# Kernel tuning notes

Hardware: AMD Instinct MI355X
Metric: run time of the kernel (lower is better)

## Reference

```python
import jax, jax.numpy as jnp
import numpy as np


def squash(t, axis=-1):
    sq = jnp.sum(t * t, axis=axis, keepdims=True)
    scale = sq / (1.0 + sq)
    return scale * t / jnp.sqrt(sq + 1e-8)


def setup_inputs() -> dict:
    key = jax.random.key(0)
    k1, k2 = jax.random.split(key)
    B, in_caps, out_caps, in_dim, out_dim = 128, 2048, 32, 8, 16
    x = jax.random.normal(k1, (B, in_caps, in_dim), dtype=jnp.float32)
    W = jax.random.normal(k2, (in_caps, out_caps, in_dim, out_dim), dtype=jnp.float32)
    return {"x": x, "W": W}


def reference(x, W):
    # x: [B, in_caps, in_dim], W: [in_caps, out_caps, in_dim, out_dim]
    # u_hat: [B, in_caps, out_caps, out_dim]
    u_hat = jnp.einsum('bni,noid->bnod', x, W)
    B, in_caps, out_caps, _ = u_hat.shape
    b = jnp.zeros((B, in_caps, out_caps, 1), dtype=u_hat.dtype)
    v = None
    for i in range(3):
        c = jax.nn.softmax(b, axis=2)              # over out_caps
        s = jnp.sum(c * u_hat, axis=1)             # [B, out_caps, out_dim]
        v = squash(s)                              # [B, out_caps, out_dim]
        if i < 2:
            b = b + jnp.sum(u_hat * v[:, None], axis=-1, keepdims=True)
    return v
```

## Files before the change

### kernel.cpp

```cpp
#include <hip/hip_runtime.h>


constexpr int NC = 2048;
constexpr int OC = 32;
constexpr int OD = 16;

typedef const __attribute__((address_space(1))) void* gas1_t;
typedef __attribute__((address_space(3))) void* las3_t;

__device__ __forceinline__ void gld16(const void* g, void* l) {
    __builtin_amdgcn_global_load_lds((gas1_t)g, (las3_t)l, 16, 0, 0);
}

#define MEMFENCE() asm volatile("" ::: "memory")
#define BAR() do { MEMFENCE(); __builtin_amdgcn_s_barrier(); MEMFENCE(); } while (0)

template<bool FIRST, bool ATOMIC>
__global__ __launch_bounds__(256)
__attribute__((amdgpu_waves_per_eu(2, 2)))
void caps_pass(const float* __restrict__ xg, const float* __restrict__ Wg,
               const float* __restrict__ vin, float* __restrict__ pout)
{
    __shared__ float4 Wl[2][1024];
    __shared__ float4 xl[1024];

    const int tid  = threadIdx.x;
    const int bid  = blockIdx.x;
    const int nsup = (bid & 7) | ((bid >> 6) << 3);
    const int bt   = (bid >> 3) & 7;
    const int w    = __builtin_amdgcn_readfirstlane(tid >> 6);
    const int lane = tid & 63;
    const int o    = lane & 31;
    const int h    = lane >> 5;
    const int sw   = o & 7;
    const int b0   = bt * 16 + w * 4;
    const int nbase = nsup * 32;

    const float4* Wg4 = (const float4*)Wg;
    const float4* xg4 = (const float4*)xg;

    float4 acc[4][2];
#pragma unroll
    for (int r = 0; r < 4; ++r)
#pragma unroll
        for (int qq = 0; qq < 2; ++qq) acc[r][qq] = make_float4(0.f, 0.f, 0.f, 0.f);

    float4 vr[4][2];
    if (!FIRST) {
        const float4* v4 = (const float4*)vin;
#pragma unroll
        for (int r = 0; r < 4; ++r)
#pragma unroll
            for (int qq = 0; qq < 2; ++qq)
                vr[r][qq] = v4[(size_t)(b0 + r) * 128 + o * 4 + h * 2 + qq];
    }

#pragma unroll
    for (int j = 0; j < 4; ++j) {
        const int L = tid + 256 * j;
        const int n = L >> 5, bb = (L >> 1) & 15, k = L & 1;
        gld16(&xg4[(size_t)(bt * 16 + bb) * 4096 + (size_t)(nbase + n) * 2 + k], &xl[L]);
    }
#pragma unroll
    for (int j = 0; j < 4; ++j) {
        const int L = tid + 256 * j;
        const int oo = L >> 5, cc = L & 31;
        gld16(&Wg4[(size_t)nbase * 1024 + oo * 32 + (cc ^ (oo & 7))], &Wl[0][L]);
    }

#pragma unroll 1
    for (int t = 0; t < 32; ++t) {
        if (t < 31) {
#pragma unroll
            for (int j = 0; j < 4; ++j) {
                const int L = tid + 256 * j;
                const int oo = L >> 5, cc = L & 31;
                gld16(&Wg4[(size_t)(nbase + t + 1) * 1024 + oo * 32 + (cc ^ (oo & 7))],
                      &Wl[(t + 1) & 1][L]);
            }
            asm volatile("s_waitcnt vmcnt(4)" ::: "memory");
        } else {
            asm volatile("s_waitcnt vmcnt(0)" ::: "memory");
        }
        BAR();

        float xr[4][8];
#pragma unroll
        for (int r = 0; r < 4; ++r) {
            const float4 xa = xl[t * 32 + (w * 4 + r) * 2 + 0];
            const float4 xb = xl[t * 32 + (w * 4 + r) * 2 + 1];
            xr[r][0] = xa.x; xr[r][1] = xa.y; xr[r][2] = xa.z; xr[r][3] = xa.w;
            xr[r][4] = xb.x; xr[r][5] = xb.y; xr[r][6] = xb.z; xr[r][7] = xb.w;
        }
        const float4* wrow = &Wl[t & 1][o * 32];

        if (FIRST) {
#pragma unroll
            for (int i = 0; i < 8; ++i)
#pragma unroll
                for (int qq = 0; qq < 2; ++qq) {
                    const float4 wv = wrow[(i * 4 + h * 2 + qq) ^ sw];
#pragma unroll
                    for (int r = 0; r < 4; ++r) {
                        acc[r][qq].x = fmaf(xr[r][i], wv.x, acc[r][qq].x);
                        acc[r][qq].y = fmaf(xr[r][i], wv.y, acc[r][qq].y);
                        acc[r][qq].z = fmaf(xr[r][i], wv.z, acc[r][qq].z);
                        acc[r][qq].w = fmaf(xr[r][i], wv.w, acc[r][qq].w);
                    }
                }
        } else {
            float4 u[4][2];
#pragma unroll
            for (int r = 0; r < 4; ++r)
#pragma unroll
                for (int qq = 0; qq < 2; ++qq) u[r][qq] = make_float4(0.f, 0.f, 0.f, 0.f);
#pragma unroll
            for (int i = 0; i < 8; ++i)
#pragma unroll
                for (int qq = 0; qq < 2; ++qq) {
                    const float4 wv = wrow[(i * 4 + h * 2 + qq) ^ sw];
#pragma unroll
                    for (int r = 0; r < 4; ++r) {
                        u[r][qq].x = fmaf(xr[r][i], wv.x, u[r][qq].x);
                        u[r][qq].y = fmaf(xr[r][i], wv.y, u[r][qq].y);
                        u[r][qq].z = fmaf(xr[r][i], wv.z, u[r][qq].z);
                        u[r][qq].w = fmaf(xr[r][i], wv.w, u[r][qq].w);
                    }
                }
#pragma unroll
            for (int r = 0; r < 4; ++r) {
                float tp = 0.f;
#pragma unroll
                for (int qq = 0; qq < 2; ++qq) {
                    tp = fmaf(u[r][qq].x, vr[r][qq].x, tp);
                    tp = fmaf(u[r][qq].y, vr[r][qq].y, tp);
                    tp = fmaf(u[r][qq].z, vr[r][qq].z, tp);
                    tp = fmaf(u[r][qq].w, vr[r][qq].w, tp);
                }
                const float tt = tp + __shfl_xor(tp, 32);
                const float e = __expf(tt);
                float Z = e;
                Z += __shfl_xor(Z, 1);
                Z += __shfl_xor(Z, 2);
                Z += __shfl_xor(Z, 4);
                Z += __shfl_xor(Z, 8);
                Z += __shfl_xor(Z, 16);
                const float c = e / Z;
#pragma unroll
                for (int qq = 0; qq < 2; ++qq) {
                    acc[r][qq].x = fmaf(c, u[r][qq].x, acc[r][qq].x);
                    acc[r][qq].y = fmaf(c, u[r][qq].y, acc[r][qq].y);
                    acc[r][qq].z = fmaf(c, u[r][qq].z, acc[r][qq].z);
                    acc[r][qq].w = fmaf(c, u[r][qq].w, acc[r][qq].w);
                }
            }
        }
        BAR();
    }

    const float sc = FIRST ? (1.0f / 32.0f) : 1.0f;
    if (ATOMIC) {
#pragma unroll
        for (int r = 0; r < 4; ++r) {
            float* sb = pout + (size_t)(b0 + r) * (OC * OD) + o * OD + h * 8;
#pragma unroll
            for (int qq = 0; qq < 2; ++qq) {
                atomicAdd(sb + qq * 4 + 0, acc[r][qq].x * sc);
                atomicAdd(sb + qq * 4 + 1, acc[r][qq].y * sc);
                atomicAdd(sb + qq * 4 + 2, acc[r][qq].z * sc);
                atomicAdd(sb + qq * 4 + 3, acc[r][qq].w * sc);
            }
        }
    } else {
        float4* P4 = (float4*)pout;
#pragma unroll
        for (int r = 0; r < 4; ++r) {
            const size_t base = ((size_t)(nsup * 128 + b0 + r) * 4 + h * 2) * 32 + o;
#pragma unroll
            for (int qq = 0; qq < 2; ++qq) {
                float4 v;
                v.x = acc[r][qq].x * sc; v.y = acc[r][qq].y * sc;
                v.z = acc[r][qq].z * sc; v.w = acc[r][qq].w * sc;
                P4[base + (size_t)qq * 32] = v;
            }
        }
    }
}

__global__ void reduce_squash(const float* __restrict__ P, const float* __restrict__ vprev,
                              float* __restrict__ vout)
{
    __shared__ float sqb[256];
    const int tid = threadIdx.x;
    const int blk = blockIdx.x;
    const float4* P4 = (const float4*)P;

    float4 a = make_float4(0.f, 0.f, 0.f, 0.f);
#pragma unroll 4
    for (int ns = 0; ns < 64; ++ns) {
        const float4 p = P4[(size_t)ns * 16384 + blk * 256 + tid];
        a.x += p.x; a.y += p.y; a.z += p.z; a.w += p.w;
    }
    sqb[tid] = a.x * a.x + a.y * a.y + a.z * a.z + a.w * a.w;
    __syncthreads();
    const int base = tid & 0x9F;
    const float sq = sqb[base] + sqb[base + 32] + sqb[base + 64] + sqb[base + 96];
    const float f = sq / ((1.0f + sq) * sqrtf(sq + 1e-8f));

    const int b  = blk * 2 + (tid >> 7);
    const int hq = (tid >> 5) & 3;
    const int o  = tid & 31;
    const size_t unit = (size_t)(b * 32 + o) * 4 + hq;
    float4 r;
    r.x = a.x * f; r.y = a.y * f; r.z = a.z * f; r.w = a.w * f;
    if (vprev) {
        const float4 p = ((const float4*)vprev)[unit];
        r.x += p.x; r.y += p.y; r.z += p.z; r.w += p.w;
    }
    ((float4*)vout)[unit] = r;
}

__global__ void squash_k(const float* __restrict__ s, const float* __restrict__ vprev,
                         float* __restrict__ vout)
{
    const int row = blockIdx.x * blockDim.x + threadIdx.x;
    if (row >= 128 * 32) return;
    const float4* s4 = (const float4*)s;
    float4 t[4];
    float sq = 0.f;
#pragma unroll
    for (int q = 0; q < 4; ++q) {
        t[q] = s4[row * 4 + q];
        sq += t[q].x * t[q].x + t[q].y * t[q].y + t[q].z * t[q].z + t[q].w * t[q].w;
    }
    const float f = sq / ((1.0f + sq) * sqrtf(sq + 1e-8f));
    float4* o4 = (float4*)vout;
#pragma unroll
    for (int q = 0; q < 4; ++q) {
        float4 r;
        r.x = t[q].x * f; r.y = t[q].y * f; r.z = t[q].z * f; r.w = t[q].w * f;
        if (vprev) {
            const float4 p = ((const float4*)vprev)[row * 4 + q];
            r.x += p.x; r.y += p.y; r.z += p.z; r.w += p.w;
        }
        o4[row * 4 + q] = r;
    }
}

extern "C" void kernel_launch(void* const* d_in, const int* in_sizes, int n_in,
                              void* d_out, int out_size, void* d_ws, size_t ws_size,
                              hipStream_t stream)
{
    const float* x = (const float*)d_in[0];
    const float* W = (const float*)d_in[1];
    float* out = (float*)d_out;

    const size_t P_FLOATS = (size_t)64 * 128 * 4 * 32 * 4;
    const size_t NEED = (P_FLOATS + 2 * 65536) * sizeof(float);

    if (ws_size >= NEED) {
        float* P  = (float*)d_ws;
        float* v0 = P + P_FLOATS;
        float* vs = v0 + 65536;

        caps_pass<true, false><<<dim3(512), dim3(256), 0, stream>>>(x, W, nullptr, P);
        reduce_squash<<<dim3(64), dim3(256), 0, stream>>>(P, nullptr, v0);

        caps_pass<false, false><<<dim3(512), dim3(256), 0, stream>>>(x, W, v0, P);
        reduce_squash<<<dim3(64), dim3(256), 0, stream>>>(P, v0, vs);

        caps_pass<false, false><<<dim3(512), dim3(256), 0, stream>>>(x, W, vs, P);
        reduce_squash<<<dim3(64), dim3(256), 0, stream>>>(P, nullptr, out);
    } else {
        float* s  = (float*)d_ws;
        float* v0 = s + 65536;
        float* vs = v0 + 65536;
        const size_t sbytes = (size_t)65536 * sizeof(float);

        hipMemsetAsync(s, 0, sbytes, stream);
        caps_pass<true, true><<<dim3(512), dim3(256), 0, stream>>>(x, W, nullptr, s);
        squash_k<<<dim3(16), dim3(256), 0, stream>>>(s, nullptr, v0);

        hipMemsetAsync(s, 0, sbytes, stream);
        caps_pass<false, true><<<dim3(512), dim3(256), 0, stream>>>(x, W, v0, s);
        squash_k<<<dim3(16), dim3(256), 0, stream>>>(s, v0, vs);

        hipMemsetAsync(s, 0, sbytes, stream);
        caps_pass<false, true><<<dim3(512), dim3(256), 0, stream>>>(x, W, vs, s);
        squash_k<<<dim3(16), dim3(256), 0, stream>>>(s, nullptr, out);
    }
}
```

Measured before the change: 195.3 us.

## Split input-capsule loop across two wave groups with LDS reduction

Doubles the block to 512 threads, with the two halves of the waves each processing alternate input capsules from a 4-deep W ring buffer. This halves the per-wave serial loop length and doubles the waves in flight, aiming to hide LDS/global latency. Partial accumulators are combined through LDS scratch before the store. This adds an extra barrier per iteration, a final reduction, higher LDS use and removes the waves_per_eu hint. The reduce kernel's unroll also goes from 4 to 8.

```diff
diff --git a/kernel.cpp b/kernel.cpp
--- a/kernel.cpp
+++ b/kernel.cpp
@@ -16,12 +16,11 @@
 #define BAR() do { MEMFENCE(); __builtin_amdgcn_s_barrier(); MEMFENCE(); } while (0)
 
 template<bool FIRST, bool ATOMIC>
-__global__ __launch_bounds__(256)
-__attribute__((amdgpu_waves_per_eu(2, 2)))
+__global__ __launch_bounds__(512)
 void caps_pass(const float* __restrict__ xg, const float* __restrict__ Wg,
                const float* __restrict__ vin, float* __restrict__ pout)
 {
-    __shared__ float4 Wl[2][1024];
+    __shared__ float4 Wl[4][1024];
     __shared__ float4 xl[1024];
 
     const int tid  = threadIdx.x;
@@ -29,11 +28,13 @@
     const int nsup = (bid & 7) | ((bid >> 6) << 3);
     const int bt   = (bid >> 3) & 7;
     const int w    = __builtin_amdgcn_readfirstlane(tid >> 6);
+    const int wg   = w & 3;
+    const int par  = w >> 2;
     const int lane = tid & 63;
     const int o    = lane & 31;
     const int h    = lane >> 5;
     const int sw   = o & 7;
-    const int b0   = bt * 16 + w * 4;
+    const int b0   = bt * 16 + wg * 4;
     const int nbase = nsup * 32;
 
     const float4* Wg4 = (const float4*)Wg;
@@ -56,27 +57,31 @@
     }
 
 #pragma unroll
-    for (int j = 0; j < 4; ++j) {
-        const int L = tid + 256 * j;
+    for (int j = 0; j < 2; ++j) {
+        const int L = tid + 512 * j;
         const int n = L >> 5, bb = (L >> 1) & 15, k = L & 1;
         gld16(&xg4[(size_t)(bt * 16 + bb) * 4096 + (size_t)(nbase + n) * 2 + k], &xl[L]);
     }
 #pragma unroll
     for (int j = 0; j < 4; ++j) {
-        const int L = tid + 256 * j;
-        const int oo = L >> 5, cc = L & 31;
-        gld16(&Wg4[(size_t)nbase * 1024 + oo * 32 + (cc ^ (oo & 7))], &Wl[0][L]);
+        const int L = tid + 512 * j;
+        const int cn = L >> 10, u = L & 1023;
+        const int oo = u >> 5, cc = u & 31;
+        gld16(&Wg4[(size_t)(nbase + cn) * 1024 + oo * 32 + (cc ^ (oo & 7))], &Wl[cn][u]);
     }
 
 #pragma unroll 1
-    for (int t = 0; t < 32; ++t) {
-        if (t < 31) {
+    for (int s = 0; s < 16; ++s) {
+        BAR();
+        if (s < 15) {
+            const int c0 = 2 * (s + 1);
 #pragma unroll
             for (int j = 0; j < 4; ++j) {
-                const int L = tid + 256 * j;
-                const int oo = L >> 5, cc = L & 31;
-                gld16(&Wg4[(size_t)(nbase + t + 1) * 1024 + oo * 32 + (cc ^ (oo & 7))],
-                      &Wl[(t + 1) & 1][L]);
+                const int L = tid + 512 * j;
+                const int cn = L >> 10, u = L & 1023;
+                const int oo = u >> 5, cc = u & 31;
+                gld16(&Wg4[(size_t)(nbase + c0 + cn) * 1024 + oo * 32 + (cc ^ (oo & 7))],
+                      &Wl[(c0 + cn) & 3][u]);
             }
             asm volatile("s_waitcnt vmcnt(4)" ::: "memory");
         } else {
@@ -84,15 +89,16 @@
         }
         BAR();
 
+        const int t = 2 * s + par;
         float xr[4][8];
 #pragma unroll
         for (int r = 0; r < 4; ++r) {
-            const float4 xa = xl[t * 32 + (w * 4 + r) * 2 + 0];
-            const float4 xb = xl[t * 32 + (w * 4 + r) * 2 + 1];
+            const float4 xa = xl[t * 32 + (wg * 4 + r) * 2 + 0];
+            const float4 xb = xl[t * 32 + (wg * 4 + r) * 2 + 1];
             xr[r][0] = xa.x; xr[r][1] = xa.y; xr[r][2] = xa.z; xr[r][3] = xa.w;
             xr[r][4] = xb.x; xr[r][5] = xb.y; xr[r][6] = xb.z; xr[r][7] = xb.w;
         }
-        const float4* wrow = &Wl[t & 1][o * 32];
+        const float4* wrow = &Wl[t & 3][o * 32];
 
         if (FIRST) {
 #pragma unroll
@@ -155,33 +161,51 @@
                 }
             }
         }
-        BAR();
-    }
-
-    const float sc = FIRST ? (1.0f / 32.0f) : 1.0f;
-    if (ATOMIC) {
-#pragma unroll
-        for (int r = 0; r < 4; ++r) {
-            float* sb = pout + (size_t)(b0 + r) * (OC * OD) + o * OD + h * 8;
+    }
+
+    BAR();
+    float4* scratch = (float4*)Wl;
+    if (par == 1) {
+#pragma unroll
+        for (int r = 0; r < 4; ++r)
+#pragma unroll
+            for (int qq = 0; qq < 2; ++qq)
+                scratch[wg * 512 + lane * 8 + ((r * 2 + qq) ^ (lane & 7))] = acc[r][qq];
+        asm volatile("s_waitcnt lgkmcnt(0)" ::: "memory");
+    }
+    BAR();
+    if (par == 0) {
+        const float sc = FIRST ? (1.0f / 32.0f) : 1.0f;
+#pragma unroll
+        for (int r = 0; r < 4; ++r)
 #pragma unroll
             for (int qq = 0; qq < 2; ++qq) {
-                atomicAdd(sb + qq * 4 + 0, acc[r][qq].x * sc);
-                atomicAdd(sb + qq * 4 + 1, acc[r][qq].y * sc);
-                atomicAdd(sb + qq * 4 + 2, acc[r][qq].z * sc);
-                atomicAdd(sb + qq * 4 + 3, acc[r][qq].w * sc);
-            }
-        }
-    } else {
-        float4* P4 = (float4*)pout;
-#pragma unroll
-        for (int r = 0; r < 4; ++r) {
-            const size_t base = ((size_t)(nsup * 128 + b0 + r) * 4 + h * 2) * 32 + o;
-#pragma unroll
-            for (int qq = 0; qq < 2; ++qq) {
-                float4 v;
-                v.x = acc[r][qq].x * sc; v.y = acc[r][qq].y * sc;
-                v.z = acc[r][qq].z * sc; v.w = acc[r][qq].w * sc;
-                P4[base + (size_t)qq * 32] = v;
+                const float4 p = scratch[wg * 512 + lane * 8 + ((r * 2 + qq) ^ (lane & 7))];
+                acc[r][qq].x = (acc[r][qq].x + p.x) * sc;
+                acc[r][qq].y = (acc[r][qq].y + p.y) * sc;
+                acc[r][qq].z = (acc[r][qq].z + p.z) * sc;
+                acc[r][qq].w = (acc[r][qq].w + p.w) * sc;
+            }
+        if (ATOMIC) {
+#pragma unroll
+            for (int r = 0; r < 4; ++r) {
+                float* sb = pout + (size_t)(b0 + r) * (OC * OD) + o * OD + h * 8;
+#pragma unroll
+                for (int qq = 0; qq < 2; ++qq) {
+                    atomicAdd(sb + qq * 4 + 0, acc[r][qq].x);
+                    atomicAdd(sb + qq * 4 + 1, acc[r][qq].y);
+                    atomicAdd(sb + qq * 4 + 2, acc[r][qq].z);
+                    atomicAdd(sb + qq * 4 + 3, acc[r][qq].w);
+                }
+            }
+        } else {
+            float4* P4 = (float4*)pout;
+#pragma unroll
+            for (int r = 0; r < 4; ++r) {
+                const size_t base = ((size_t)(nsup * 128 + b0 + r) * 4 + h * 2) * 32 + o;
+#pragma unroll
+                for (int qq = 0; qq < 2; ++qq)
+                    P4[base + (size_t)qq * 32] = acc[r][qq];
             }
         }
     }
@@ -196,7 +220,7 @@
     const float4* P4 = (const float4*)P;
 
     float4 a = make_float4(0.f, 0.f, 0.f, 0.f);
-#pragma unroll 4
+#pragma unroll 8
     for (int ns = 0; ns < 64; ++ns) {
         const float4 p = P4[(size_t)ns * 16384 + blk * 256 + tid];
         a.x += p.x; a.y += p.y; a.z += p.z; a.w += p.w;
@@ -263,13 +287,13 @@
         float* v0 = P + P_FLOATS;
         float* vs = v0 + 65536;
 
-        caps_pass<true, false><<<dim3(512), dim3(256), 0, stream>>>(x, W, nullptr, P);
+        caps_pass<true, false><<<dim3(512), dim3(512), 0, stream>>>(x, W, nullptr, P);
         reduce_squash<<<dim3(64), dim3(256), 0, stream>>>(P, nullptr, v0);
 
-        caps_pass<false, false><<<dim3(512), dim3(256), 0, stream>>>(x, W, v0, P);
+        caps_pass<false, false><<<dim3(512), dim3(512), 0, stream>>>(x, W, v0, P);
         reduce_squash<<<dim3(64), dim3(256), 0, stream>>>(P, v0, vs);
 
-        caps_pass<false, false><<<dim3(512), dim3(256), 0, stream>>>(x, W, vs, P);
+        caps_pass<false, false><<<dim3(512), dim3(512), 0, stream>>>(x, W, vs, P);
         reduce_squash<<<dim3(64), dim3(256), 0, stream>>>(P, nullptr, out);
     } else {
         float* s  = (float*)d_ws;
@@ -278,15 +302,15 @@
         const size_t sbytes = (size_t)65536 * sizeof(float);
 
         hipMemsetAsync(s, 0, sbytes, stream);
-        caps_pass<true, true><<<dim3(512), dim3(256), 0, stream>>>(x, W, nullptr, s);
+        caps_pass<true, true><<<dim3(512), dim3(512), 0, stream>>>(x, W, nullptr, s);
         squash_k<<<dim3(16), dim3(256), 0, stream>>>(s, nullptr, v0);
 
         hipMemsetAsync(s, 0, sbytes, stream);
-        caps_pass<false, true><<<dim3(512), dim3(256), 0, stream>>>(x, W, v0, s);
+        caps_pass<false, true><<<dim3(512), dim3(512), 0, stream>>>(x, W, v0, s);
         squash_k<<<dim3(16), dim3(256), 0, stream>>>(s, v0, vs);
 
         hipMemsetAsync(s, 0, sbytes, stream);
-        caps_pass<false, true><<<dim3(512), dim3(256), 0, stream>>>(x, W, vs, s);
+        caps_pass<false, true><<<dim3(512), dim3(512), 0, stream>>>(x, W, vs, s);
         squash_k<<<dim3(16), dim3(256), 0, stream>>>(s, nullptr, out);
     }
 }
```

Measured after the change: 214.5 us. +9.9%, slower.

## Halve capsules per block, read x directly from global, reprioritize waves

Applied to the files above, without the earlier changes.

Templates the capsule pass on capsules-per-block (NR=16), doubling the grid to 1024 blocks with a wider partial-sum buffer and a 128-way reduction. The x tile is no longer staged in LDS and is read per thread from global memory. The barrier is moved to the top of each iteration, s_setprio raises wave priority during the FMA phase, and the fixed waves_per_eu attribute is dropped. The aim is more occupancy and parallelism, at the cost of more partial-sum traffic and uncoalesced x loads.

```diff
diff --git a/kernel.cpp b/kernel.cpp
--- a/kernel.cpp
+++ b/kernel.cpp
@@ -15,29 +15,27 @@
 #define MEMFENCE() asm volatile("" ::: "memory")
 #define BAR() do { MEMFENCE(); __builtin_amdgcn_s_barrier(); MEMFENCE(); } while (0)
 
-template<bool FIRST, bool ATOMIC>
+template<int NR, bool FIRST, bool ATOMIC>
 __global__ __launch_bounds__(256)
-__attribute__((amdgpu_waves_per_eu(2, 2)))
 void caps_pass(const float* __restrict__ xg, const float* __restrict__ Wg,
                const float* __restrict__ vin, float* __restrict__ pout)
 {
     __shared__ float4 Wl[2][1024];
-    __shared__ float4 xl[1024];
-
+
+    constexpr int NSUPC = 2048 / NR;
     const int tid  = threadIdx.x;
     const int bid  = blockIdx.x;
-    const int nsup = (bid & 7) | ((bid >> 6) << 3);
-    const int bt   = (bid >> 3) & 7;
+    const int bt   = bid / NSUPC;
+    const int nsup = bid % NSUPC;
     const int w    = __builtin_amdgcn_readfirstlane(tid >> 6);
     const int lane = tid & 63;
     const int o    = lane & 31;
     const int h    = lane >> 5;
     const int sw   = o & 7;
     const int b0   = bt * 16 + w * 4;
-    const int nbase = nsup * 32;
+    const int nbase = nsup * NR;
 
     const float4* Wg4 = (const float4*)Wg;
-    const float4* xg4 = (const float4*)xg;
 
     float4 acc[4][2];
 #pragma unroll
@@ -55,12 +53,6 @@
                 vr[r][qq] = v4[(size_t)(b0 + r) * 128 + o * 4 + h * 2 + qq];
     }
 
-#pragma unroll
-    for (int j = 0; j < 4; ++j) {
-        const int L = tid + 256 * j;
-        const int n = L >> 5, bb = (L >> 1) & 15, k = L & 1;
-        gld16(&xg4[(size_t)(bt * 16 + bb) * 4096 + (size_t)(nbase + n) * 2 + k], &xl[L]);
-    }
 #pragma unroll
     for (int j = 0; j < 4; ++j) {
         const int L = tid + 256 * j;
@@ -69,8 +61,9 @@
     }
 
 #pragma unroll 1
-    for (int t = 0; t < 32; ++t) {
-        if (t < 31) {
+    for (int t = 0; t < NR; ++t) {
+        BAR();
+        if (t + 1 < NR) {
 #pragma unroll
             for (int j = 0; j < 4; ++j) {
                 const int L = tid + 256 * j;
@@ -84,16 +77,17 @@
         }
         BAR();
 
-        float xr[4][8];
+        const int n = nbase + t;
+        float xs[4][8];
 #pragma unroll
         for (int r = 0; r < 4; ++r) {
-            const float4 xa = xl[t * 32 + (w * 4 + r) * 2 + 0];
-            const float4 xb = xl[t * 32 + (w * 4 + r) * 2 + 1];
-            xr[r][0] = xa.x; xr[r][1] = xa.y; xr[r][2] = xa.z; xr[r][3] = xa.w;
-            xr[r][4] = xb.x; xr[r][5] = xb.y; xr[r][6] = xb.z; xr[r][7] = xb.w;
+            const float* xp = xg + ((size_t)(b0 + r) * NC + n) * 8;
+#pragma unroll
+            for (int i = 0; i < 8; ++i) xs[r][i] = xp[i];
         }
         const float4* wrow = &Wl[t & 1][o * 32];
 
+        __builtin_amdgcn_s_setprio(1);
         if (FIRST) {
 #pragma unroll
             for (int i = 0; i < 8; ++i)
@@ -102,10 +96,10 @@
                     const float4 wv = wrow[(i * 4 + h * 2 + qq) ^ sw];
 #pragma unroll
                     for (int r = 0; r < 4; ++r) {
-                        acc[r][qq].x = fmaf(xr[r][i], wv.x, acc[r][qq].x);
-                        acc[r][qq].y = fmaf(xr[r][i], wv.y, acc[r][qq].y);
-                        acc[r][qq].z = fmaf(xr[r][i], wv.z, acc[r][qq].z);
-                        acc[r][qq].w = fmaf(xr[r][i], wv.w, acc[r][qq].w);
+                        acc[r][qq].x = fmaf(xs[r][i], wv.x, acc[r][qq].x);
+                        acc[r][qq].y = fmaf(xs[r][i], wv.y, acc[r][qq].y);
+                        acc[r][qq].z = fmaf(xs[r][i], wv.z, acc[r][qq].z);
+                        acc[r][qq].w = fmaf(xs[r][i], wv.w, acc[r][qq].w);
                     }
                 }
         } else {
@@ -121,10 +115,10 @@
                     const float4 wv = wrow[(i * 4 + h * 2 + qq) ^ sw];
 #pragma unroll
                     for (int r = 0; r < 4; ++r) {
-                        u[r][qq].x = fmaf(xr[r][i], wv.x, u[r][qq].x);
-                        u[r][qq].y = fmaf(xr[r][i], wv.y, u[r][qq].y);
-                        u[r][qq].z = fmaf(xr[r][i], wv.z, u[r][qq].z);
-                        u[r][qq].w = fmaf(xr[r][i], wv.w, u[r][qq].w);
+                        u[r][qq].x = fmaf(xs[r][i], wv.x, u[r][qq].x);
+                        u[r][qq].y = fmaf(xs[r][i], wv.y, u[r][qq].y);
+                        u[r][qq].z = fmaf(xs[r][i], wv.z, u[r][qq].z);
+                        u[r][qq].w = fmaf(xs[r][i], wv.w, u[r][qq].w);
                     }
                 }
 #pragma unroll
@@ -155,7 +149,7 @@
                 }
             }
         }
-        BAR();
+        __builtin_amdgcn_s_setprio(0);
     }
 
     const float sc = FIRST ? (1.0f / 32.0f) : 1.0f;
@@ -187,6 +181,7 @@
     }
 }
 
+template<int NS>
 __global__ void reduce_squash(const float* __restrict__ P, const float* __restrict__ vprev,
                               float* __restrict__ vout)
 {
@@ -196,8 +191,8 @@
     const float4* P4 = (const float4*)P;
 
     float4 a = make_float4(0.f, 0.f, 0.f, 0.f);
-#pragma unroll 4
-    for (int ns = 0; ns < 64; ++ns) {
+#pragma unroll 8
+    for (int ns = 0; ns < NS; ++ns) {
         const float4 p = P4[(size_t)ns * 16384 + blk * 256 + tid];
         a.x += p.x; a.y += p.y; a.z += p.z; a.w += p.w;
     }
@@ -255,22 +250,37 @@
     const float* W = (const float*)d_in[1];
     float* out = (float*)d_out;
 
-    const size_t P_FLOATS = (size_t)64 * 128 * 4 * 32 * 4;
-    const size_t NEED = (P_FLOATS + 2 * 65536) * sizeof(float);
-
-    if (ws_size >= NEED) {
+    const size_t P1 = (size_t)128 * 128 * 512;
+    const size_t P2 = (size_t)64 * 128 * 512;
+    const size_t NEED1 = (P1 + 2 * 65536) * sizeof(float);
+    const size_t NEED2 = (P2 + 2 * 65536) * sizeof(float);
+
+    if (ws_size >= NEED1) {
         float* P  = (float*)d_ws;
-        float* v0 = P + P_FLOATS;
+        float* v0 = P + P1;
         float* vs = v0 + 65536;
 
-        caps_pass<true, false><<<dim3(512), dim3(256), 0, stream>>>(x, W, nullptr, P);
-        reduce_squash<<<dim3(64), dim3(256), 0, stream>>>(P, nullptr, v0);
-
-        caps_pass<false, false><<<dim3(512), dim3(256), 0, stream>>>(x, W, v0, P);
-        reduce_squash<<<dim3(64), dim3(256), 0, stream>>>(P, v0, vs);
-
-        caps_pass<false, false><<<dim3(512), dim3(256), 0, stream>>>(x, W, vs, P);
-        reduce_squash<<<dim3(64), dim3(256), 0, stream>>>(P, nullptr, out);
+        caps_pass<16, true, false><<<dim3(1024), dim3(256), 0, stream>>>(x, W, nullptr, P);
+        reduce_squash<128><<<dim3(64), dim3(256), 0, stream>>>(P, nullptr, v0);
+
+        caps_pass<16, false, false><<<dim3(1024), dim3(256), 0, stream>>>(x, W, v0, P);
+        reduce_squash<128><<<dim3(64), dim3(256), 0, stream>>>(P, v0, vs);
+
+        caps_pass<16, false, false><<<dim3(1024), dim3(256), 0, stream>>>(x, W, vs, P);
+        reduce_squash<128><<<dim3(64), dim3(256), 0, stream>>>(P, nullptr, out);
+    } else if (ws_size >= NEED2) {
+        float* P  = (float*)d_ws;
+        float* v0 = P + P2;
+        float* vs = v0 + 65536;
+
+        caps_pass<32, true, false><<<dim3(512), dim3(256), 0, stream>>>(x, W, nullptr, P);
+        reduce_squash<64><<<dim3(64), dim3(256), 0, stream>>>(P, nullptr, v0);
+
+        caps_pass<32, false, false><<<dim3(512), dim3(256), 0, stream>>>(x, W, v0, P);
+        reduce_squash<64><<<dim3(64), dim3(256), 0, stream>>>(P, v0, vs);
+
+        caps_pass<32, false, false><<<dim3(512), dim3(256), 0, stream>>>(x, W, vs, P);
+        reduce_squash<64><<<dim3(64), dim3(256), 0, stream>>>(P, nullptr, out);
     } else {
         float* s  = (float*)d_ws;
         float* v0 = s + 65536;
@@ -278,15 +288,15 @@
         const size_t sbytes = (size_t)65536 * sizeof(float);
 
         hipMemsetAsync(s, 0, sbytes, stream);
-        caps_pass<true, true><<<dim3(512), dim3(256), 0, stream>>>(x, W, nullptr, s);
+        caps_pass<16, true, true><<<dim3(1024), dim3(256), 0, stream>>>(x, W, nullptr, s);
         squash_k<<<dim3(16), dim3(256), 0, stream>>>(s, nullptr, v0);
 
         hipMemsetAsync(s, 0, sbytes, stream);
-        caps_pass<false, true><<<dim3(512), dim3(256), 0, stream>>>(x, W, v0, s);
+        caps_pass<16, false, true><<<dim3(1024), dim3(256), 0, stream>>>(x, W, v0, s);
         squash_k<<<dim3(16), dim3(256), 0, stream>>>(s, v0, vs);
 
         hipMemsetAsync(s, 0, sbytes, stream);
-        caps_pass<false, true><<<dim3(512), dim3(256), 0, stream>>>(x, W, vs, s);
+        caps_pass<16, false, true><<<dim3(1024), dim3(256), 0, stream>>>(x, W, vs, s);
         squash_k<<<dim3(16), dim3(256), 0, stream>>>(s, nullptr, out);
     }
 }
```

Result: no change. 195.5 us (+0.1%).
